# Kernel tuning notes

Hardware: AMD Instinct MI355X
Metric: run time of the kernel (lower is better)

## Reference

```python
import jax, jax.numpy as jnp
import numpy as np

# pywt 'db4' decomposition filters (8 taps)
DEC_LO = jnp.array([-0.010597401784997278, 0.032883011666982945, 0.030841381835986965,
                    -0.18703481171888114, -0.02798376941698385, 0.6308807679295904,
                    0.7148465705525415, 0.23037781330885523], dtype=jnp.float32)
DEC_HI = jnp.array([-0.23037781330885523, 0.7148465705525415, -0.6308807679295904,
                    -0.02798376941698385, 0.18703481171888114, 0.030841381835986965,
                    -0.032883011666982945, -0.010597401784997278], dtype=jnp.float32)
LEVELS = 3


def _dwt_step(sig, lo, hi):
    """One pywt dwt level, mode='symmetric'. sig: [M, S] -> (cA, cD) each [M, (S+F-1)//2]."""
    F = lo.shape[0]
    # symmetric extension by F-1 on each side; drop first sample so stride-2
    # correlation picks the odd-indexed valid-convolution outputs (pywt convention)
    ext = jnp.pad(sig, ((0, 0), (F - 1, F - 1)), mode='symmetric')[:, 1:]
    # true convolution = correlation with flipped filters
    kern = jnp.stack([lo[::-1], hi[::-1]])[:, None, :]          # [2, 1, F]
    y = jax.lax.conv_general_dilated(ext[:, None, :], kern, (2,), 'VALID')  # [M, 2, out]
    return y[:, 0], y[:, 1]


def _resize(c, T):
    """Match torch: truncate if longer than T, else F.interpolate linear align_corners=False."""
    S = c.shape[-1]
    if S == T:
        return c
    if S > T:
        return c[..., :T]
    pos = (jnp.arange(T, dtype=c.dtype) + 0.5) * (S / T) - 0.5
    pos = jnp.clip(pos, 0.0, S - 1)
    lo = jnp.floor(pos).astype(jnp.int32)
    hi = jnp.minimum(lo + 1, S - 1)
    w = pos - lo.astype(c.dtype)
    return c[..., lo] * (1.0 - w) + c[..., hi] * w


def setup_inputs() -> dict:
    key = jax.random.key(0)
    x = jax.random.normal(key, (16, 2048, 512, 1), dtype=jnp.float32)
    return {"x": x}


def reference(x):
    B, T, N, _ = x.shape
    sig = x[:, :, :, 0].transpose(0, 2, 1).reshape(B * N, T)  # [B*N, T]
    a = sig
    details = []
    for _ in range(LEVELS):
        a, d = _dwt_step(a, DEC_LO, DEC_HI)
        details.append(d)
    coeffs = [a] + details[::-1]  # pywt order: [cA_L, cD_L, ..., cD_1]
    out = jnp.stack([_resize(c, T) for c in coeffs], axis=-1)  # [B*N, T, L+1]
    return out.reshape(B, N, T, LEVELS + 1)
```

## Files before the change

kernel.cpp:

```cpp
#include <hip/hip_runtime.h>


#define TPB   512
#define ROWS  4
#define TLEN  2048
#define NCH   512
#define RSTRIDE 4104
#define CA1_OFF 2048
#define CD1_OFF 3075
#define CA2_OFF 0
#define CD2_OFF 517
#define CA3_OFF 1034
#define CD3_OFF 1296

typedef float f32x4 __attribute__((ext_vector_type(4)));

__constant__ float LO[8] = {-0.010597401784997278f,  0.032883011666982945f,  0.030841381835986965f,
                            -0.18703481171888114f,  -0.02798376941698385f,   0.6308807679295904f,
                             0.7148465705525415f,    0.23037781330885523f};
__constant__ float HI[8] = {-0.23037781330885523f,   0.7148465705525415f,   -0.6308807679295904f,
                            -0.02798376941698385f,   0.18703481171888114f,   0.030841381835986965f,
                            -0.032883011666982945f, -0.010597401784997278f};
__constant__ float RLO[8] = { 0.23037781330885523f,   0.7148465705525415f,   0.6308807679295904f,
                             -0.02798376941698385f,  -0.18703481171888114f,  0.030841381835986965f,
                              0.032883011666982945f, -0.010597401784997278f};
__constant__ float RHI[8] = {-0.010597401784997278f, -0.032883011666982945f, 0.030841381835986965f,
                              0.18703481171888114f,  -0.02798376941698385f,  -0.6308807679295904f,
                              0.7148465705525415f,   -0.23037781330885523f};

__device__ __forceinline__ int sym_idx(int e, int S) {
    int m = e - 6;
    m = (m < 0) ? (-1 - m) : m;
    m = (m >= S) ? (2 * S - 1 - m) : m;
    return m;
}

__device__ __forceinline__ void dwt_level(float* lds, int in_off, int S,
                                          int lo_off, int hi_off, int tid) {
    const int O    = (S + 7) >> 1;
    const int jmax = (S - 2) >> 1;
    const int NI   = jmax - 2;
    const int NB   = O - NI;

    for (int i = tid; i < ROWS * NI; i += TPB) {
        const int r = i & 3;
        const int j = (i >> 2) + 3;
        float* rowp = lds + r * RSTRIDE;
        const float* p = rowp + in_off + 2 * j - 6;
        float v[8];
        *(float2*)&v[0] = ((const float2*)p)[0];
        *(float2*)&v[2] = ((const float2*)p)[1];
        *(float2*)&v[4] = ((const float2*)p)[2];
        *(float2*)&v[6] = ((const float2*)p)[3];
        float slo = 0.0f, shi = 0.0f;
        #pragma unroll
        for (int k = 0; k < 8; ++k) {
            slo = fmaf(RLO[k], v[k], slo);
            shi = fmaf(RHI[k], v[k], shi);
        }
        rowp[lo_off + j] = slo;
        rowp[hi_off + j] = shi;
    }
    for (int i = tid; i < ROWS * NB; i += TPB) {
        const int r  = i & 3;
        const int bj = i >> 2;
        const int j  = (bj < 3) ? bj : (jmax + bj - 2);
        float* rowp = lds + r * RSTRIDE;
        const float* in = rowp + in_off;
        float slo = 0.0f, shi = 0.0f;
        const int e0 = 2 * j + 7;
        #pragma unroll
        for (int k = 0; k < 8; ++k) {
            const float v = in[sym_idx(e0 - k, S)];
            slo = fmaf(LO[k], v, slo);
            shi = fmaf(HI[k], v, shi);
        }
        rowp[lo_off + j] = slo;
        rowp[hi_off + j] = shi;
    }
}

__device__ __forceinline__ void lerp_coef(int S, int t, int& i0, int& i1, float& w) {
    const float scale = (float)S * (1.0f / 2048.0f);
    float p = ((float)t + 0.5f) * scale - 0.5f;
    p = fminf(fmaxf(p, 0.0f), (float)(S - 1));
    i0 = (int)p;
    i1 = min(i0 + 1, S - 1);
    w = p - (float)i0;
}

__device__ __forceinline__ float mix2(float a, float b, float w) {
    return a * (1.0f - w) + b * w;
}

__global__ __launch_bounds__(TPB)
void dwt_kernel(const float* __restrict__ x, float* __restrict__ out) {
    __shared__ float lds[ROWS * RSTRIDE];
    const int tid = threadIdx.x;

    const int nwg   = gridDim.x;
    const int chunk = nwg >> 3;
    const int p     = blockIdx.x;
    const int bid   = (p & 7) * chunk + (p >> 3);

    const int row0 = bid * ROWS;
    const int b    = row0 >> 9;
    const int n0   = row0 & 511;

    const float4* src = (const float4*)(x + (size_t)b * TLEN * NCH + n0);
    #pragma unroll
    for (int t = tid; t < TLEN; t += TPB) {
        const float4 v = src[t * (NCH / 4)];
        lds[0 * RSTRIDE + t] = v.x;
        lds[1 * RSTRIDE + t] = v.y;
        lds[2 * RSTRIDE + t] = v.z;
        lds[3 * RSTRIDE + t] = v.w;
    }
    __syncthreads();

    dwt_level(lds, 0,       2048, CA1_OFF, CD1_OFF, tid);
    __syncthreads();
    dwt_level(lds, CA1_OFF, 1027, CA2_OFF, CD2_OFF, tid);
    __syncthreads();
    dwt_level(lds, CA2_OFF,  517, CA3_OFF, CD3_OFF, tid);
    __syncthreads();

    f32x4* dst = (f32x4*)out + (size_t)row0 * TLEN;
    #pragma unroll
    for (int t = tid; t < TLEN; t += TPB) {
        int i0a, i1a; float wa; lerp_coef( 262, t, i0a, i1a, wa);
        int i0b, i1b; float wb; lerp_coef( 517, t, i0b, i1b, wb);
        int i0c, i1c; float wc; lerp_coef(1027, t, i0c, i1c, wc);
        #pragma unroll
        for (int r = 0; r < ROWS; ++r) {
            const float* rowp = lds + r * RSTRIDE;
            f32x4 o;
            o.x = mix2(rowp[CA3_OFF + i0a], rowp[CA3_OFF + i1a], wa);
            o.y = mix2(rowp[CD3_OFF + i0a], rowp[CD3_OFF + i1a], wa);
            o.z = mix2(rowp[CD2_OFF + i0b], rowp[CD2_OFF + i1b], wb);
            o.w = mix2(rowp[CD1_OFF + i0c], rowp[CD1_OFF + i1c], wc);
            __builtin_nontemporal_store(o, &dst[r * TLEN + t]);
        }
    }
}

extern "C" void kernel_launch(void* const* d_in, const int* in_sizes, int n_in,
                              void* d_out, int out_size, void* d_ws, size_t ws_size,
                              hipStream_t stream) {
    const float* x = (const float*)d_in[0];
    float* out = (float*)d_out;
    const int n_rows = 16 * 512;
    dim3 grid(n_rows / ROWS), block(TPB);
    hipLaunchKernelGGL(dwt_kernel, grid, block, 0, stream, x, out);
}
```

Baseline: 60.93 us.

## Process multiple row tiles per block with register prefetch of next tile

Each workgroup now handles four consecutive 4-row tiles instead of one, so the grid shrinks to 512 blocks. While the current tile's DWT levels and interpolated output run from LDS, the next tile's global loads are issued into registers, then written to LDS after a barrier. Plain __syncthreads are replaced with an lgkmcnt wait plus s_barrier. The goal is to hide global load latency behind compute and stores. The cost is fewer blocks for parallelism, more registers held live, and extra barriers.

```diff
diff --git a/kernel.cpp b/kernel.cpp
--- a/kernel.cpp
+++ b/kernel.cpp
@@ -3,6 +3,7 @@
 
 #define TPB   512
 #define ROWS  4
+#define NTILE 4
 #define TLEN  2048
 #define NCH   512
 #define RSTRIDE 4104
@@ -27,6 +28,11 @@
 __constant__ float RHI[8] = {-0.010597401784997278f, -0.032883011666982945f, 0.030841381835986965f,
                               0.18703481171888114f,  -0.02798376941698385f,  -0.6308807679295904f,
                               0.7148465705525415f,   -0.23037781330885523f};
+
+__device__ __forceinline__ void bar_lgkm() {
+    asm volatile("s_waitcnt lgkmcnt(0)" ::: "memory");
+    __builtin_amdgcn_s_barrier();
+}
 
 __device__ __forceinline__ int sym_idx(int e, int S) {
     int m = e - 6;
@@ -98,48 +104,71 @@
     __shared__ float lds[ROWS * RSTRIDE];
     const int tid = threadIdx.x;
 
-    const int nwg   = gridDim.x;
-    const int chunk = nwg >> 3;
     const int p     = blockIdx.x;
-    const int bid   = (p & 7) * chunk + (p >> 3);
+    const int tile0 = (p & 7) * 256 + (p >> 3) * NTILE;
 
-    const int row0 = bid * ROWS;
-    const int b    = row0 >> 9;
-    const int n0   = row0 & 511;
+    float4 pre[4];
 
-    const float4* src = (const float4*)(x + (size_t)b * TLEN * NCH + n0);
+    {
+        const int row0 = tile0 * ROWS;
+        const float4* src = (const float4*)(x + (size_t)(row0 >> 9) * TLEN * NCH + (row0 & 511));
+        #pragma unroll
+        for (int i = 0; i < 4; ++i) pre[i] = src[(tid + i * TPB) * (NCH / 4)];
+    }
     #pragma unroll
-    for (int t = tid; t < TLEN; t += TPB) {
-        const float4 v = src[t * (NCH / 4)];
-        lds[0 * RSTRIDE + t] = v.x;
-        lds[1 * RSTRIDE + t] = v.y;
-        lds[2 * RSTRIDE + t] = v.z;
-        lds[3 * RSTRIDE + t] = v.w;
+    for (int i = 0; i < 4; ++i) {
+        const int t = tid + i * TPB;
+        lds[0 * RSTRIDE + t] = pre[i].x;
+        lds[1 * RSTRIDE + t] = pre[i].y;
+        lds[2 * RSTRIDE + t] = pre[i].z;
+        lds[3 * RSTRIDE + t] = pre[i].w;
     }
-    __syncthreads();
+    bar_lgkm();
 
-    dwt_level(lds, 0,       2048, CA1_OFF, CD1_OFF, tid);
-    __syncthreads();
-    dwt_level(lds, CA1_OFF, 1027, CA2_OFF, CD2_OFF, tid);
-    __syncthreads();
-    dwt_level(lds, CA2_OFF,  517, CA3_OFF, CD3_OFF, tid);
-    __syncthreads();
+    for (int k = 0; k < NTILE; ++k) {
+        const int row0 = (tile0 + k) * ROWS;
 
-    f32x4* dst = (f32x4*)out + (size_t)row0 * TLEN;
-    #pragma unroll
-    for (int t = tid; t < TLEN; t += TPB) {
-        int i0a, i1a; float wa; lerp_coef( 262, t, i0a, i1a, wa);
-        int i0b, i1b; float wb; lerp_coef( 517, t, i0b, i1b, wb);
-        int i0c, i1c; float wc; lerp_coef(1027, t, i0c, i1c, wc);
+        if (k + 1 < NTILE) {
+            const int nrow0 = row0 + ROWS;
+            const float4* nsrc = (const float4*)(x + (size_t)(nrow0 >> 9) * TLEN * NCH + (nrow0 & 511));
+            #pragma unroll
+            for (int i = 0; i < 4; ++i) pre[i] = nsrc[(tid + i * TPB) * (NCH / 4)];
+            __builtin_amdgcn_sched_barrier(0);
+        }
+
+        dwt_level(lds, 0,       2048, CA1_OFF, CD1_OFF, tid);  bar_lgkm();
+        dwt_level(lds, CA1_OFF, 1027, CA2_OFF, CD2_OFF, tid);  bar_lgkm();
+        dwt_level(lds, CA2_OFF,  517, CA3_OFF, CD3_OFF, tid);  bar_lgkm();
+
+        f32x4* dst = (f32x4*)out + (size_t)row0 * TLEN;
         #pragma unroll
-        for (int r = 0; r < ROWS; ++r) {
-            const float* rowp = lds + r * RSTRIDE;
-            f32x4 o;
-            o.x = mix2(rowp[CA3_OFF + i0a], rowp[CA3_OFF + i1a], wa);
-            o.y = mix2(rowp[CD3_OFF + i0a], rowp[CD3_OFF + i1a], wa);
-            o.z = mix2(rowp[CD2_OFF + i0b], rowp[CD2_OFF + i1b], wb);
-            o.w = mix2(rowp[CD1_OFF + i0c], rowp[CD1_OFF + i1c], wc);
-            __builtin_nontemporal_store(o, &dst[r * TLEN + t]);
+        for (int t = tid; t < TLEN; t += TPB) {
+            int i0a, i1a; float wa; lerp_coef( 262, t, i0a, i1a, wa);
+            int i0b, i1b; float wb; lerp_coef( 517, t, i0b, i1b, wb);
+            int i0c, i1c; float wc; lerp_coef(1027, t, i0c, i1c, wc);
+            #pragma unroll
+            for (int r = 0; r < ROWS; ++r) {
+                const float* rowp = lds + r * RSTRIDE;
+                f32x4 o;
+                o.x = mix2(rowp[CA3_OFF + i0a], rowp[CA3_OFF + i1a], wa);
+                o.y = mix2(rowp[CD3_OFF + i0a], rowp[CD3_OFF + i1a], wa);
+                o.z = mix2(rowp[CD2_OFF + i0b], rowp[CD2_OFF + i1b], wb);
+                o.w = mix2(rowp[CD1_OFF + i0c], rowp[CD1_OFF + i1c], wc);
+                __builtin_nontemporal_store(o, &dst[r * TLEN + t]);
+            }
+        }
+
+        if (k + 1 < NTILE) {
+            bar_lgkm();
+            #pragma unroll
+            for (int i = 0; i < 4; ++i) {
+                const int t = tid + i * TPB;
+                lds[0 * RSTRIDE + t] = pre[i].x;
+                lds[1 * RSTRIDE + t] = pre[i].y;
+                lds[2 * RSTRIDE + t] = pre[i].z;
+                lds[3 * RSTRIDE + t] = pre[i].w;
+            }
+            bar_lgkm();
         }
     }
 }
@@ -149,7 +178,7 @@
                               hipStream_t stream) {
     const float* x = (const float*)d_in[0];
     float* out = (float*)d_out;
-    const int n_rows = 16 * 512;
-    dim3 grid(n_rows / ROWS), block(TPB);
+    const int n_blocks = 16 * 512 / (ROWS * NTILE);
+    dim3 grid(n_blocks), block(TPB);
     hipLaunchKernelGGL(dwt_kernel, grid, block, 0, stream, x, out);
 }
```

Measured after the change: 88.59 us. 1.45x slower.

## Assign one wavefront per row and compute DWT levels in place without barriers

Applied to the files above, without the earlier changes.

Each of four wavefronts now owns one signal row. It runs all three DWT levels on that row with wave-synchronous LDS access, which removes the block-wide __syncthreads between levels. The approximation coefficients are written in place over the input region, so the per-row LDS footprint shrinks from 4104 to 3080 floats. Block size drops from 512 to 256 threads. The cost is serial per-row work inside each wave and a reliance on in-wave ordering for the in-place overwrite being safe, while the kernel stays dominated by its large output write traffic.

```diff
diff --git a/kernel.cpp b/kernel.cpp
--- a/kernel.cpp
+++ b/kernel.cpp
@@ -1,17 +1,15 @@
 #include <hip/hip_runtime.h>
 
 
-#define TPB   512
+#define TPB   256
 #define ROWS  4
 #define TLEN  2048
 #define NCH   512
-#define RSTRIDE 4104
-#define CA1_OFF 2048
-#define CD1_OFF 3075
-#define CA2_OFF 0
-#define CD2_OFF 517
-#define CA3_OFF 1034
-#define CD3_OFF 1296
+#define RSTRIDE 3080
+#define CA3_OFF 0
+#define CD3_OFF 520
+#define CD2_OFF 1027
+#define CD1_OFF 2048
 
 typedef float f32x4 __attribute__((ext_vector_type(4)));
 
@@ -35,45 +33,33 @@
     return m;
 }
 
-__device__ __forceinline__ void dwt_level(float* lds, int in_off, int S,
-                                          int lo_off, int hi_off, int tid) {
+__device__ __forceinline__ void dwt_level_wave(float* rowp, int in_off, int S,
+                                               int lo_off, int hi_off, int lane) {
     const int O    = (S + 7) >> 1;
     const int jmax = (S - 2) >> 1;
-    const int NI   = jmax - 2;
-    const int NB   = O - NI;
-
-    for (int i = tid; i < ROWS * NI; i += TPB) {
-        const int r = i & 3;
-        const int j = (i >> 2) + 3;
-        float* rowp = lds + r * RSTRIDE;
-        const float* p = rowp + in_off + 2 * j - 6;
-        float v[8];
-        *(float2*)&v[0] = ((const float2*)p)[0];
-        *(float2*)&v[2] = ((const float2*)p)[1];
-        *(float2*)&v[4] = ((const float2*)p)[2];
-        *(float2*)&v[6] = ((const float2*)p)[3];
+    for (int j = lane; j < O; j += 64) {
         float slo = 0.0f, shi = 0.0f;
-        #pragma unroll
-        for (int k = 0; k < 8; ++k) {
-            slo = fmaf(RLO[k], v[k], slo);
-            shi = fmaf(RHI[k], v[k], shi);
-        }
-        rowp[lo_off + j] = slo;
-        rowp[hi_off + j] = shi;
-    }
-    for (int i = tid; i < ROWS * NB; i += TPB) {
-        const int r  = i & 3;
-        const int bj = i >> 2;
-        const int j  = (bj < 3) ? bj : (jmax + bj - 2);
-        float* rowp = lds + r * RSTRIDE;
-        const float* in = rowp + in_off;
-        float slo = 0.0f, shi = 0.0f;
-        const int e0 = 2 * j + 7;
-        #pragma unroll
-        for (int k = 0; k < 8; ++k) {
-            const float v = in[sym_idx(e0 - k, S)];
-            slo = fmaf(LO[k], v, slo);
-            shi = fmaf(HI[k], v, shi);
+        if (j >= 3 && j <= jmax) {
+            const float* p = rowp + in_off + 2 * j - 6;
+            float v[8];
+            *(float2*)&v[0] = ((const float2*)p)[0];
+            *(float2*)&v[2] = ((const float2*)p)[1];
+            *(float2*)&v[4] = ((const float2*)p)[2];
+            *(float2*)&v[6] = ((const float2*)p)[3];
+            #pragma unroll
+            for (int k = 0; k < 8; ++k) {
+                slo = fmaf(RLO[k], v[k], slo);
+                shi = fmaf(RHI[k], v[k], shi);
+            }
+        } else {
+            const float* in = rowp + in_off;
+            const int e0 = 2 * j + 7;
+            #pragma unroll
+            for (int k = 0; k < 8; ++k) {
+                const float v = in[sym_idx(e0 - k, S)];
+                slo = fmaf(LO[k], v, slo);
+                shi = fmaf(HI[k], v, shi);
+            }
         }
         rowp[lo_off + j] = slo;
         rowp[hi_off + j] = shi;
@@ -109,7 +95,8 @@
 
     const float4* src = (const float4*)(x + (size_t)b * TLEN * NCH + n0);
     #pragma unroll
-    for (int t = tid; t < TLEN; t += TPB) {
+    for (int i = 0; i < TLEN / TPB; ++i) {
+        const int t = tid + i * TPB;
         const float4 v = src[t * (NCH / 4)];
         lds[0 * RSTRIDE + t] = v.x;
         lds[1 * RSTRIDE + t] = v.y;
@@ -118,29 +105,27 @@
     }
     __syncthreads();
 
-    dwt_level(lds, 0,       2048, CA1_OFF, CD1_OFF, tid);
-    __syncthreads();
-    dwt_level(lds, CA1_OFF, 1027, CA2_OFF, CD2_OFF, tid);
-    __syncthreads();
-    dwt_level(lds, CA2_OFF,  517, CA3_OFF, CD3_OFF, tid);
-    __syncthreads();
+    const int wave = tid >> 6;
+    const int lane = tid & 63;
+    float* rowp = lds + wave * RSTRIDE;
 
-    f32x4* dst = (f32x4*)out + (size_t)row0 * TLEN;
-    #pragma unroll
-    for (int t = tid; t < TLEN; t += TPB) {
+    dwt_level_wave(rowp, 0, 2048, 0, CD1_OFF, lane);
+    dwt_level_wave(rowp, 0, 1027, 0, CD2_OFF, lane);
+    dwt_level_wave(rowp, 0,  517, 0, CD3_OFF, lane);
+
+    f32x4* dst = (f32x4*)out + (size_t)(row0 + wave) * TLEN;
+    #pragma unroll 4
+    for (int i = 0; i < TLEN / 64; ++i) {
+        const int t = lane + i * 64;
         int i0a, i1a; float wa; lerp_coef( 262, t, i0a, i1a, wa);
         int i0b, i1b; float wb; lerp_coef( 517, t, i0b, i1b, wb);
         int i0c, i1c; float wc; lerp_coef(1027, t, i0c, i1c, wc);
-        #pragma unroll
-        for (int r = 0; r < ROWS; ++r) {
-            const float* rowp = lds + r * RSTRIDE;
-            f32x4 o;
-            o.x = mix2(rowp[CA3_OFF + i0a], rowp[CA3_OFF + i1a], wa);
-            o.y = mix2(rowp[CD3_OFF + i0a], rowp[CD3_OFF + i1a], wa);
-            o.z = mix2(rowp[CD2_OFF + i0b], rowp[CD2_OFF + i1b], wb);
-            o.w = mix2(rowp[CD1_OFF + i0c], rowp[CD1_OFF + i1c], wc);
-            __builtin_nontemporal_store(o, &dst[r * TLEN + t]);
-        }
+        f32x4 o;
+        o.x = mix2(rowp[CA3_OFF + i0a], rowp[CA3_OFF + i1a], wa);
+        o.y = mix2(rowp[CD3_OFF + i0a], rowp[CD3_OFF + i1a], wa);
+        o.z = mix2(rowp[CD2_OFF + i0b], rowp[CD2_OFF + i1b], wb);
+        o.w = mix2(rowp[CD1_OFF + i0c], rowp[CD1_OFF + i1c], wc);
+        __builtin_nontemporal_store(o, &dst[t]);
     }
 }
 
```

New measurement: 66.08 us. +8.5%, slower.

## Use persistent warp-specialized blocks with double-buffered producer loads

Applied to the files above, without the earlier changes.

The launch is replaced with 256 persistent blocks, each handling 8 four-row tiles. Each block gets 128 loader threads that prefetch the next tile from global memory into a double-buffered LDS input while 512 compute threads run the three DWT levels and the resize output on the current tile. The aim is to hide the strided global-load latency behind compute, at the cost of more LDS per block, fewer resident blocks, and a fixed barrier protocol that must match between the two thread groups. The tile-to-block mapping is hardcoded to 256 blocks, and the LDS layout is reorganised so level outputs reuse the input buffer.

```diff
diff --git a/kernel.cpp b/kernel.cpp
--- a/kernel.cpp
+++ b/kernel.cpp
@@ -1,17 +1,21 @@
 #include <hip/hip_runtime.h>
 
 
-#define TPB   512
-#define ROWS  4
-#define TLEN  2048
-#define NCH   512
-#define RSTRIDE 4104
-#define CA1_OFF 2048
-#define CD1_OFF 3075
-#define CA2_OFF 0
-#define CD2_OFF 517
-#define CA3_OFF 1034
-#define CD3_OFF 1296
+#define TPB      640
+#define CTHREADS 512
+#define LTHREADS 128
+#define ROWS     4
+#define NT       8
+#define TLEN     2048
+#define NCH      512
+#define IBSTRIDE 2088
+#define SCSTRIDE 2056
+#define CA1_OFF  0
+#define CD1_OFF  1028
+#define CA2_OFF  0
+#define CD2_OFF  520
+#define CA3_OFF  1040
+#define CD3_OFF  1304
 
 typedef float f32x4 __attribute__((ext_vector_type(4)));
 
@@ -28,6 +32,11 @@
                               0.18703481171888114f,  -0.02798376941698385f,  -0.6308807679295904f,
                               0.7148465705525415f,   -0.23037781330885523f};
 
+__device__ __forceinline__ void bar_lgkm() {
+    asm volatile("s_waitcnt lgkmcnt(0)" ::: "memory");
+    __builtin_amdgcn_s_barrier();
+}
+
 __device__ __forceinline__ int sym_idx(int e, int S) {
     int m = e - 6;
     m = (m < 0) ? (-1 - m) : m;
@@ -35,18 +44,18 @@
     return m;
 }
 
-__device__ __forceinline__ void dwt_level(float* lds, int in_off, int S,
+__device__ __forceinline__ void dwt_level(const float* inb, int instride, int S,
+                                          float* outb, int outstride,
                                           int lo_off, int hi_off, int tid) {
     const int O    = (S + 7) >> 1;
     const int jmax = (S - 2) >> 1;
     const int NI   = jmax - 2;
     const int NB   = O - NI;
 
-    for (int i = tid; i < ROWS * NI; i += TPB) {
+    for (int i = tid; i < ROWS * NI; i += CTHREADS) {
         const int r = i & 3;
         const int j = (i >> 2) + 3;
-        float* rowp = lds + r * RSTRIDE;
-        const float* p = rowp + in_off + 2 * j - 6;
+        const float* p = inb + r * instride + 2 * j - 6;
         float v[8];
         *(float2*)&v[0] = ((const float2*)p)[0];
         *(float2*)&v[2] = ((const float2*)p)[1];
@@ -58,15 +67,15 @@
             slo = fmaf(RLO[k], v[k], slo);
             shi = fmaf(RHI[k], v[k], shi);
         }
-        rowp[lo_off + j] = slo;
-        rowp[hi_off + j] = shi;
+        float* orow = outb + r * outstride;
+        orow[lo_off + j] = slo;
+        orow[hi_off + j] = shi;
     }
-    for (int i = tid; i < ROWS * NB; i += TPB) {
+    for (int i = tid; i < ROWS * NB; i += CTHREADS) {
         const int r  = i & 3;
         const int bj = i >> 2;
         const int j  = (bj < 3) ? bj : (jmax + bj - 2);
-        float* rowp = lds + r * RSTRIDE;
-        const float* in = rowp + in_off;
+        const float* in = inb + r * instride;
         float slo = 0.0f, shi = 0.0f;
         const int e0 = 2 * j + 7;
         #pragma unroll
@@ -75,8 +84,9 @@
             slo = fmaf(LO[k], v, slo);
             shi = fmaf(HI[k], v, shi);
         }
-        rowp[lo_off + j] = slo;
-        rowp[hi_off + j] = shi;
+        float* orow = outb + r * outstride;
+        orow[lo_off + j] = slo;
+        orow[hi_off + j] = shi;
     }
 }
 
@@ -93,53 +103,90 @@
     return a * (1.0f - w) + b * w;
 }
 
+__device__ __forceinline__ int tile_row0(int p, int j) {
+    const int tile = (p & 7) * 256 + (p >> 3) + 32 * j;
+    return tile * ROWS;
+}
+
 __global__ __launch_bounds__(TPB)
 void dwt_kernel(const float* __restrict__ x, float* __restrict__ out) {
-    __shared__ float lds[ROWS * RSTRIDE];
+    __shared__ float ib[2][ROWS][IBSTRIDE];
+    __shared__ float sc[ROWS][SCSTRIDE];
     const int tid = threadIdx.x;
-
-    const int nwg   = gridDim.x;
-    const int chunk = nwg >> 3;
-    const int p     = blockIdx.x;
-    const int bid   = (p & 7) * chunk + (p >> 3);
-
-    const int row0 = bid * ROWS;
-    const int b    = row0 >> 9;
-    const int n0   = row0 & 511;
-
-    const float4* src = (const float4*)(x + (size_t)b * TLEN * NCH + n0);
-    #pragma unroll
-    for (int t = tid; t < TLEN; t += TPB) {
-        const float4 v = src[t * (NCH / 4)];
-        lds[0 * RSTRIDE + t] = v.x;
-        lds[1 * RSTRIDE + t] = v.y;
-        lds[2 * RSTRIDE + t] = v.z;
-        lds[3 * RSTRIDE + t] = v.w;
-    }
-    __syncthreads();
-
-    dwt_level(lds, 0,       2048, CA1_OFF, CD1_OFF, tid);
-    __syncthreads();
-    dwt_level(lds, CA1_OFF, 1027, CA2_OFF, CD2_OFF, tid);
-    __syncthreads();
-    dwt_level(lds, CA2_OFF,  517, CA3_OFF, CD3_OFF, tid);
-    __syncthreads();
-
-    f32x4* dst = (f32x4*)out + (size_t)row0 * TLEN;
-    #pragma unroll
-    for (int t = tid; t < TLEN; t += TPB) {
-        int i0a, i1a; float wa; lerp_coef( 262, t, i0a, i1a, wa);
-        int i0b, i1b; float wb; lerp_coef( 517, t, i0b, i1b, wb);
-        int i0c, i1c; float wc; lerp_coef(1027, t, i0c, i1c, wc);
-        #pragma unroll
-        for (int r = 0; r < ROWS; ++r) {
-            const float* rowp = lds + r * RSTRIDE;
-            f32x4 o;
-            o.x = mix2(rowp[CA3_OFF + i0a], rowp[CA3_OFF + i1a], wa);
-            o.y = mix2(rowp[CD3_OFF + i0a], rowp[CD3_OFF + i1a], wa);
-            o.z = mix2(rowp[CD2_OFF + i0b], rowp[CD2_OFF + i1b], wb);
-            o.w = mix2(rowp[CD1_OFF + i0c], rowp[CD1_OFF + i1c], wc);
-            __builtin_nontemporal_store(o, &dst[r * TLEN + t]);
+    const int p   = blockIdx.x;
+
+    if (tid >= CTHREADS) {
+        const int lt = tid - CTHREADS;
+        float4 pre[16];
+
+        #define LOAD_TILE(J) {                                                        \
+            const int row0 = tile_row0(p, (J));                                       \
+            const float4* s = (const float4*)(x + (size_t)(row0 >> 9) * TLEN * NCH    \
+                                                + (row0 & 511));                      \
+            _Pragma("unroll")                                                         \
+            for (int i = 0; i < 16; ++i) pre[i] = s[(lt + i * LTHREADS) * (NCH / 4)]; }
+
+        #define WRITE_TILE(BUF) {                                                     \
+            _Pragma("unroll")                                                         \
+            for (int i = 0; i < 16; ++i) {                                            \
+                const int t = lt + i * LTHREADS;                                      \
+                ib[(BUF)][0][t] = pre[i].x;                                           \
+                ib[(BUF)][1][t] = pre[i].y;                                           \
+                ib[(BUF)][2][t] = pre[i].z;                                           \
+                ib[(BUF)][3][t] = pre[i].w;                                           \
+            } }
+
+        LOAD_TILE(0);
+        WRITE_TILE(0);
+        LOAD_TILE(1);
+        bar_lgkm();
+
+        for (int j = 0; j < NT; ++j) {
+            if (j + 1 < NT) WRITE_TILE((j + 1) & 1);
+            bar_lgkm();
+            if (j + 2 < NT) LOAD_TILE(j + 2);
+            bar_lgkm();
+            bar_lgkm();
+            bar_lgkm();
+        }
+        #undef LOAD_TILE
+        #undef WRITE_TILE
+    } else {
+        bar_lgkm();
+
+        for (int j = 0; j < NT; ++j) {
+            float (*ibc)[IBSTRIDE] = ib[j & 1];
+            const int row0 = tile_row0(p, j);
+
+            dwt_level(&ibc[0][0], IBSTRIDE, 2048,
+                      &sc[0][0],  SCSTRIDE, CA1_OFF, CD1_OFF, tid);
+            bar_lgkm();
+            dwt_level(&sc[0][0] + CA1_OFF, SCSTRIDE, 1027,
+                      &ibc[0][0], IBSTRIDE, CA2_OFF, CD2_OFF, tid);
+            bar_lgkm();
+            dwt_level(&ibc[0][0] + CA2_OFF, IBSTRIDE, 517,
+                      &ibc[0][0], IBSTRIDE, CA3_OFF, CD3_OFF, tid);
+            bar_lgkm();
+
+            f32x4* dst = (f32x4*)out + (size_t)row0 * TLEN;
+            #pragma unroll
+            for (int t = tid; t < TLEN; t += CTHREADS) {
+                int i0a, i1a; float wa; lerp_coef( 262, t, i0a, i1a, wa);
+                int i0b, i1b; float wb; lerp_coef( 517, t, i0b, i1b, wb);
+                int i0c, i1c; float wc; lerp_coef(1027, t, i0c, i1c, wc);
+                #pragma unroll
+                for (int r = 0; r < ROWS; ++r) {
+                    const float* irow = &ibc[r][0];
+                    const float* srow = &sc[r][0];
+                    f32x4 o;
+                    o.x = mix2(irow[CA3_OFF + i0a], irow[CA3_OFF + i1a], wa);
+                    o.y = mix2(irow[CD3_OFF + i0a], irow[CD3_OFF + i1a], wa);
+                    o.z = mix2(irow[CD2_OFF + i0b], irow[CD2_OFF + i1b], wb);
+                    o.w = mix2(srow[CD1_OFF + i0c], srow[CD1_OFF + i1c], wc);
+                    __builtin_nontemporal_store(o, &dst[r * TLEN + t]);
+                }
+            }
+            bar_lgkm();
         }
     }
 }
@@ -149,7 +196,6 @@
                               hipStream_t stream) {
     const float* x = (const float*)d_in[0];
     float* out = (float*)d_out;
-    const int n_rows = 16 * 512;
-    dim3 grid(n_rows / ROWS), block(TPB);
+    dim3 grid(256), block(TPB);
     hipLaunchKernelGGL(dwt_kernel, grid, block, 0, stream, x, out);
 }
```

Result: no change. 61.81 us (+1.4%).
